# Optimization experiments

Hardware: AMD Instinct MI355X
Metric: run time of the kernel (lower is better)

Reference implementation:

```python
import jax, jax.numpy as jnp
import numpy as np

B, L = 32, 200
NUM_C, NUM_D, DIM_V = 256, 32, 128


def setup_inputs() -> dict:
    key = jax.random.key(0)
    ks = jax.random.split(key, 20)
    def n(k, shape, s=0.05):
        return (jax.random.normal(k, shape) * s).astype(jnp.float32)
    return {
        "c_seq": jax.random.randint(ks[0], (B, L), 0, NUM_C),
        "d_seq": jax.random.randint(ks[1], (B, L), 0, NUM_D),
        "r_seq": jax.random.uniform(ks[2], (B, L), dtype=jnp.float32),
        # learned params
        "X": n(ks[3], (NUM_C * NUM_D, DIM_V), 0.1),      # Embedding table
        "v_r": n(ks[4], (DIM_V,), 0.1),
        "v_beta": n(ks[5], (DIM_V,), 0.1),
        # GRU (torch layout: gates [r|z|n] stacked)
        "W_ih": n(ks[6], (3 * DIM_V, 2 * DIM_V)),
        "W_hh": n(ks[7], (3 * DIM_V, DIM_V)),
        "b_ih": n(ks[8], (3 * DIM_V,)),
        "b_hh": n(ks[9], (3 * DIM_V,)),
        # linear_1: dim_v -> dim_v -> num_d (dropout = identity in eval)
        "W1a": n(ks[10], (DIM_V, DIM_V)), "b1a": n(ks[11], (DIM_V,)),
        "W1b": n(ks[12], (NUM_D, DIM_V)), "b1b": n(ks[13], (NUM_D,)),
        # linear_2: 3*dim_v -> dim_v -> num_d
        "W2a": n(ks[14], (DIM_V, 3 * DIM_V)), "b2a": n(ks[15], (DIM_V,)),
        "W2b": n(ks[16], (NUM_D, DIM_V)), "b2b": n(ks[17], (NUM_D,)),
    }


def reference(c_seq, d_seq, r_seq, X, v_r, v_beta, W_ih, W_hh, b_ih, b_hh,
              W1a, b1a, W1b, b1b, W2a, b2a, W2b, b2b):
    # embedding lookup: x = c + num_c * d
    v_x_seq = X[c_seq + NUM_C * d_seq]              # [B,L,V]
    v_r_seq = r_seq[..., None] * v_r                # [B,L,V]
    gru_in = jnp.concatenate([v_x_seq, v_r_seq], -1)  # [B,L,2V]

    # GRU (torch semantics), precompute input projections
    gx = jnp.einsum('blf,gf->blg', gru_in, W_ih) + b_ih  # [B,L,3V]

    def gru_step(h, gx_t):
        gh = h @ W_hh.T + b_hh
        xr, xz, xn = jnp.split(gx_t, 3, axis=-1)
        hr, hz, hn = jnp.split(gh, 3, axis=-1)
        r = jax.nn.sigmoid(xr + hr)
        z = jax.nn.sigmoid(xz + hz)
        n_ = jnp.tanh(xn + r * hn)
        h = (1.0 - z) * n_ + z * h
        return h, h

    h0 = jnp.zeros((B, DIM_V), dtype=gru_in.dtype)
    _, h_seq = jax.lax.scan(gru_step, h0, jnp.swapaxes(gx, 0, 1))
    h_seq = jnp.swapaxes(h_seq, 0, 1)               # [B,L,V]

    # linear_1 (dropout is identity at inference)
    alpha_seq = jax.nn.relu(h_seq @ W1a.T + b1a) @ W1b.T + b1b  # [B,L,num_d]

    # sequential memory update; one-hot gather/scatter expressed as true
    # gather C[b, c_t, d_t] and row scatter C[b, c_t, :] = new_c (same math)
    bidx = jnp.arange(B)

    def mem_step(C, inp):
        c_t, d_t, vx_t, vr_t = inp
        beta = C[bidx, c_t, d_t]                    # [B]
        v_beta_t = beta[:, None] * v_beta           # [B,V]
        zcat = jnp.concatenate([v_beta_t, vx_t, vr_t], -1)  # [B,3V]
        new_c = jax.nn.relu(zcat @ W2a.T + b2a) @ W2b.T + b2b  # [B,num_d]
        C = C.at[bidx, c_t].set(new_c)
        return C, C

    C0 = jnp.zeros((B, NUM_C, NUM_D), jnp.float32)
    _, C_seq = jax.lax.scan(
        mem_step, C0,
        (jnp.swapaxes(c_seq, 0, 1), jnp.swapaxes(d_seq, 0, 1),
         jnp.swapaxes(v_x_seq, 0, 1), jnp.swapaxes(v_r_seq, 0, 1)))
    C_seq = jnp.swapaxes(C_seq, 0, 1)               # [B,L,num_c,num_d]
    return alpha_seq, h_seq, C_seq
```

## Files before the change

### kernel.cpp

```cpp
#include <hip/hip_runtime.h>
#include <hip/hip_bf16.h>

typedef unsigned short u16;
typedef unsigned int u32;
typedef short short8 __attribute__((ext_vector_type(8)));
typedef float f32x4 __attribute__((ext_vector_type(4)));

constexpr int BATCH = 32, L = 200, NUM_C = 256, NUM_D = 32, V = 128;
constexpr int G3 = 384;
constexpr int KQ = 512;
constexpr int ROWS = BATCH * L;
constexpr size_t ALPHA_OFF = 0;
constexpr size_t H_OFF = (size_t)ROWS * NUM_D;
constexpr size_t C_OFF = H_OFF + (size_t)ROWS * V;

__device__ inline u16 f2bf(float f) {
  __hip_bfloat16 h = __float2bfloat16(f);
  return __builtin_bit_cast(u16, h);
}
__device__ inline float bf2f(u16 u) { u32 x = ((u32)u) << 16; return __builtin_bit_cast(float, x); }

__device__ inline void cvt32(const float* __restrict__ src, u16* __restrict__ dst) {
#pragma unroll
  for (int j0 = 0; j0 < 32; j0 += 4) {
    const f32x4 v = *(const f32x4*)(src + j0);
    ushort4 s;
    s.x = f2bf(v[0]); s.y = f2bf(v[1]); s.z = f2bf(v[2]); s.w = f2bf(v[3]);
    *(ushort4*)(dst + j0) = s;
  }
}
__device__ inline short8 ldfrag(const float* __restrict__ p) {
  const f32x4 a = *(const f32x4*)p, b = *(const f32x4*)(p + 4);
  short8 s;
  s[0] = (short)f2bf(a[0]); s[1] = (short)f2bf(a[1]);
  s[2] = (short)f2bf(a[2]); s[3] = (short)f2bf(a[3]);
  s[4] = (short)f2bf(b[0]); s[5] = (short)f2bf(b[1]);
  s[6] = (short)f2bf(b[2]); s[7] = (short)f2bf(b[3]);
  return s;
}

__global__ __launch_bounds__(256) void k1(
    const int* __restrict__ c_seq, const int* __restrict__ d_seq,
    const float* __restrict__ r_seq, const float* __restrict__ X,
    const float* __restrict__ v_r, const float* __restrict__ W_ih,
    const float* __restrict__ W2a, const float* __restrict__ b_ih,
    const float* __restrict__ b2a, float* __restrict__ Qout)
{
  __shared__ __align__(16) u16 Als[64][144];
  __shared__ __align__(16) u16 Bls[64][144];
  const int tid = threadIdx.x;
  const int mt = blockIdx.x, nt = blockIdx.y;
  const int lane = tid & 63, w = tid >> 6;
  const int q = lane >> 4, m = lane & 15;

  f32x4 acc[4];
#pragma unroll
  for (int i = 0; i < 4; ++i) acc[i] = (f32x4)0.0f;

  const int r0 = tid >> 2;
  const int kc = (tid & 3) * 32;
  const int rowg = mt * 64 + r0;
  const int gcolB = nt * 64 + r0;

  for (int s = 0; s < 2; ++s) {
    if (s) __syncthreads();
    if (s == 0) {
      const int idx = c_seq[rowg] + NUM_C * d_seq[rowg];
      cvt32(X + (size_t)idx * V + kc, &Als[r0][kc]);
    } else {
      const float rv = r_seq[rowg];
#pragma unroll
      for (int j0 = 0; j0 < 32; j0 += 4) {
        const f32x4 v = *(const f32x4*)(v_r + kc + j0);
        ushort4 sv;
        sv.x = f2bf(rv * v[0]); sv.y = f2bf(rv * v[1]);
        sv.z = f2bf(rv * v[2]); sv.w = f2bf(rv * v[3]);
        *(ushort4*)&Als[r0][kc + j0] = sv;
      }
    }
    {
      const float* src = (gcolB < G3)
        ? (W_ih + (size_t)gcolB * 256 + s * 128 + kc)
        : (W2a + (size_t)(gcolB - G3) * G3 + V + s * 128 + kc);
      cvt32(src, &Bls[r0][kc]);
    }
    __syncthreads();
#pragma unroll
    for (int c = 0; c < 4; ++c) {
      const short8 af = *(const short8*)&Als[w * 16 + m][32 * c + 8 * q];
#pragma unroll
      for (int i = 0; i < 4; ++i) {
        const short8 bf = *(const short8*)&Bls[i * 16 + m][32 * c + 8 * q];
        acc[i] = __builtin_amdgcn_mfma_f32_16x16x32_bf16(af, bf, acc[i], 0, 0, 0);
      }
    }
  }
#pragma unroll
  for (int i = 0; i < 4; ++i) {
    const int col = nt * 64 + i * 16 + m;
    const float bias = (col < G3) ? b_ih[col] : b2a[col - G3];
#pragma unroll
    for (int r = 0; r < 4; ++r) {
      const int rowo = mt * 64 + w * 16 + q * 4 + r;
      Qout[(size_t)rowo * KQ + col] = acc[i][r] + bias;
    }
  }
}

union ShK2 {
  struct { u16 h_bf[2][V]; } g;
  struct { float C[NUM_C * NUM_D]; int cb[L]; int db[L]; float u[V]; } s;
};

__global__ __launch_bounds__(256, 1) void k2(
    const int* __restrict__ c_seq, const int* __restrict__ d_seq,
    const float* __restrict__ W_hh, const float* __restrict__ b_hh,
    const float* __restrict__ W2a, const float* __restrict__ v_beta,
    const float* __restrict__ W2b, const float* __restrict__ b2b,
    const float* __restrict__ Q, float* __restrict__ out)
{
  __shared__ __align__(16) ShK2 sh;
  const int tid = threadIdx.x;
  const int l = tid & 63, w = tid >> 6, q = l >> 4, m = l & 15;

  if (blockIdx.x < 32) {
    const int b = blockIdx.x;
    if (tid < V) sh.g.h_bf[0][tid] = 0;
    __syncthreads();
    short8 wf[6][4];
    float bhh[6]; int gcol[6];
#pragma unroll
    for (int i = 0; i < 6; ++i) {
      const int g = (w + 4 * i) * 16 + m;
      gcol[i] = g;
      bhh[i] = b_hh[g];
#pragma unroll
      for (int c = 0; c < 4; ++c)
        wf[i][c] = ldfrag(W_hh + (size_t)g * V + 32 * c + 8 * q);
    }
    const float* Qb = Q + (size_t)b * L * KQ;
    float* outh = out + H_OFF + (size_t)b * L * V;
    const int vi0 = 16 * w + m, vi1 = 64 + 16 * w + m;
    float hold[2] = {0.f, 0.f};
    float hst[2] = {0.f, 0.f};
    float gxv[6];
#pragma unroll
    for (int i = 0; i < 6; ++i) gxv[i] = Qb[gcol[i]];
    for (int t = 0; t < L; ++t) {
      const int rs = t & 1, wsl = rs ^ 1;
      short8 af[4];
#pragma unroll
      for (int c = 0; c < 4; ++c)
        af[c] = *(const short8*)&sh.g.h_bf[rs][32 * c + 8 * q];
      float gxn[6];
      const float* Qn = Qb + (size_t)((t + 1 < L) ? t + 1 : t) * KQ;
#pragma unroll
      for (int i = 0; i < 6; ++i) gxn[i] = Qn[gcol[i]];
      if (t > 0 && q == 0) {
        outh[(size_t)(t - 1) * V + vi0] = hst[0];
        outh[(size_t)(t - 1) * V + vi1] = hst[1];
      }
      f32x4 acc[6];
#pragma unroll
      for (int i = 0; i < 6; ++i) acc[i] = (f32x4)0.0f;
#pragma unroll
      for (int c = 0; c < 4; ++c)
#pragma unroll
        for (int i = 0; i < 6; ++i)
          acc[i] = __builtin_amdgcn_mfma_f32_16x16x32_bf16(af[c], wf[i][c], acc[i], 0, 0, 0);
      float hnew[2];
#pragma unroll
      for (int s = 0; s < 2; ++s) {
        const float xr = gxv[0 + s] + acc[0 + s][0] + bhh[0 + s];
        const float xz = gxv[2 + s] + acc[2 + s][0] + bhh[2 + s];
        const float ghn = acc[4 + s][0] + bhh[4 + s];
        const float r = 1.f / (1.f + __expf(-xr));
        const float z = 1.f / (1.f + __expf(-xz));
        const float xn = gxv[4 + s] + r * ghn;
        const float e = __expf(2.f * xn);
        const float n = 1.f - 2.f / (e + 1.f);
        hnew[s] = (1.f - z) * n + z * hold[s];
      }
      if (q == 0) {
        sh.g.h_bf[wsl][vi0] = f2bf(hnew[0]);
        sh.g.h_bf[wsl][vi1] = f2bf(hnew[1]);
      }
      hold[0] = hnew[0]; hold[1] = hnew[1];
      hst[0] = hnew[0]; hst[1] = hnew[1];
      __builtin_amdgcn_s_waitcnt(0xc07f);
      __builtin_amdgcn_s_barrier();
#pragma unroll
      for (int i = 0; i < 6; ++i) gxv[i] = gxn[i];
    }
    if (q == 0) {
      outh[(size_t)(L - 1) * V + vi0] = hst[0];
      outh[(size_t)(L - 1) * V + vi1] = hst[1];
    }
  } else {
    const int b = blockIdx.x - 32;
    for (int i = tid; i < NUM_C * NUM_D; i += 256) sh.s.C[i] = 0.f;
    if (tid < L) { sh.s.cb[tid] = c_seq[b * L + tid]; sh.s.db[tid] = d_seq[b * L + tid]; }
    if (tid < V) {
      float a = 0.f;
      const float* wr = W2a + (size_t)tid * G3;
      for (int k = 0; k < V; ++k) a += wr[k] * v_beta[k];
      sh.s.u[tid] = a;
    }
    __syncthreads();
    if (tid >= 64) return;
    float ureg[4][8];
#pragma unroll
    for (int c = 0; c < 4; ++c)
#pragma unroll
      for (int j = 0; j < 8; ++j) ureg[c][j] = sh.s.u[32 * c + 8 * q + j];
    short8 wbf[2][4];
    float bb[2];
#pragma unroll
    for (int tt = 0; tt < 2; ++tt) {
#pragma unroll
      for (int c = 0; c < 4; ++c)
        wbf[tt][c] = ldfrag(W2b + (size_t)(tt * 16 + m) * V + 32 * c + 8 * q);
      bb[tt] = b2b[tt * 16 + m];
    }
    const float* Pb = Q + (size_t)b * L * KQ + G3;
    float* outc = out + C_OFF + (size_t)b * L * (NUM_C * NUM_D);
    f32x4 pcur[4][2];
#pragma unroll
    for (int c = 0; c < 4; ++c) {
      pcur[c][0] = *(const f32x4*)(Pb + 32 * c + 8 * q);
      pcur[c][1] = *(const f32x4*)(Pb + 32 * c + 8 * q + 4);
    }
    float beta = 0.f;
    int ct = sh.s.cb[0];
    for (int t = 0; t < L; ++t) {
      __builtin_amdgcn_s_waitcnt(0xc07f);
      const int tn = (t + 1 < L) ? t + 1 : t;
      const int cn = sh.s.cb[tn], dn = sh.s.db[tn];
      const float bpre = sh.s.C[cn * NUM_D + dn];
      short8 af[4];
#pragma unroll
      for (int c = 0; c < 4; ++c) {
        short8 a;
#pragma unroll
        for (int j = 0; j < 8; ++j) {
          const float p = (j < 4) ? pcur[c][0][j] : pcur[c][1][j - 4];
          const float hv = fmaxf(beta * ureg[c][j] + p, 0.f);
          a[j] = (short)f2bf(hv);
        }
        af[c] = a;
      }
      const float* Pn = Pb + (size_t)tn * KQ;
#pragma unroll
      for (int c = 0; c < 4; ++c) {
        pcur[c][0] = *(const f32x4*)(Pn + 32 * c + 8 * q);
        pcur[c][1] = *(const f32x4*)(Pn + 32 * c + 8 * q + 4);
      }
      f32x4 a0 = (f32x4)0.0f, a1 = (f32x4)0.0f;
#pragma unroll
      for (int c = 0; c < 4; ++c) {
        a0 = __builtin_amdgcn_mfma_f32_16x16x32_bf16(af[c], wbf[0][c], a0, 0, 0, 0);
        a1 = __builtin_amdgcn_mfma_f32_16x16x32_bf16(af[c], wbf[1][c], a1, 0, 0, 0);
      }
      const float n0 = a0[0] + bb[0], n1 = a1[0] + bb[1];
      if (q == 0) {
        sh.s.C[ct * NUM_D + m] = n0;
        sh.s.C[ct * NUM_D + 16 + m] = n1;
        float* oc = outc + (size_t)t * (NUM_C * NUM_D) + ct * NUM_D;
        oc[m] = n0;
        oc[16 + m] = n1;
      }
      float nb = bpre;
      if (cn == ct) nb = (dn < 16) ? __shfl(n0, dn, 64) : __shfl(n1, dn - 16, 64);
      beta = nb;
      ct = cn;
    }
  }
}

union ShK3 {
  struct { int cb[L]; float stage[L][NUM_D]; } f;
  struct { u16 hls[64][144]; u16 hid[64][144]; } a;
};

__global__ __launch_bounds__(256) void k3(
    const int* __restrict__ c_seq, const float* __restrict__ W1a,
    const float* __restrict__ b1a, const float* __restrict__ W1b,
    const float* __restrict__ b1b, float* __restrict__ out)
{
  __shared__ __align__(16) ShK3 sh;
  const int tid = threadIdx.x;
  if (blockIdx.x < 256) {
    const int blk = blockIdx.x;
    const int b = blk >> 3, cbase = (blk & 7) * 32;
    if (tid < L) sh.f.cb[tid] = c_seq[b * L + tid];
    __syncthreads();
    if (tid < L) {
      const int c = sh.f.cb[tid];
      if (c >= cbase && c < cbase + 32) {
        const float* src = out + C_OFF + ((size_t)b * L + tid) * (NUM_C * NUM_D) + (size_t)c * NUM_D;
#pragma unroll
        for (int j = 0; j < 8; ++j)
          *(f32x4*)&sh.f.stage[tid][j * 4] = *(const f32x4*)(src + j * 4);
      }
    }
    __syncthreads();
    const int cl = tid >> 3, dq = (tid & 7) * 4;
    const int myc = cbase + cl;
    float* base = out + C_OFF + (size_t)b * L * (NUM_C * NUM_D) + (size_t)myc * NUM_D + dq;
    f32x4 cur = (f32x4)0.0f;
    for (int t = 0; t < L; ++t) {
      if (sh.f.cb[t] == myc) cur = *(const f32x4*)&sh.f.stage[t][dq];
      *(f32x4*)base = cur;
      base += NUM_C * NUM_D;
    }
  } else {
    const int ab = blockIdx.x - 256;
    const int l = tid & 63, w = tid >> 6, q = l >> 4, m = l & 15;
    {
      const int r0 = tid >> 2, kc = (tid & 3) * 32;
      cvt32(out + H_OFF + (size_t)(ab * 64 + r0) * V + kc, &sh.a.hls[r0][kc]);
    }
    __syncthreads();
    f32x4 acc1[8];
#pragma unroll
    for (int i = 0; i < 8; ++i) acc1[i] = (f32x4)0.0f;
#pragma unroll
    for (int c = 0; c < 4; ++c) {
      const short8 af = *(const short8*)&sh.a.hls[w * 16 + m][32 * c + 8 * q];
#pragma unroll
      for (int i = 0; i < 8; ++i) {
        const short8 bf = ldfrag(W1a + (size_t)(i * 16 + m) * V + 32 * c + 8 * q);
        acc1[i] = __builtin_amdgcn_mfma_f32_16x16x32_bf16(af, bf, acc1[i], 0, 0, 0);
      }
    }
#pragma unroll
    for (int i = 0; i < 8; ++i) {
      const int col = i * 16 + m;
      const float bias = b1a[col];
#pragma unroll
      for (int r = 0; r < 4; ++r)
        sh.a.hid[w * 16 + q * 4 + r][col] = f2bf(fmaxf(acc1[i][r] + bias, 0.f));
    }
    __syncthreads();
    f32x4 acc2[2];
    acc2[0] = (f32x4)0.0f; acc2[1] = (f32x4)0.0f;
#pragma unroll
    for (int c = 0; c < 4; ++c) {
      const short8 af = *(const short8*)&sh.a.hid[w * 16 + m][32 * c + 8 * q];
#pragma unroll
      for (int tt = 0; tt < 2; ++tt) {
        const short8 bf = ldfrag(W1b + (size_t)(tt * 16 + m) * V + 32 * c + 8 * q);
        acc2[tt] = __builtin_amdgcn_mfma_f32_16x16x32_bf16(af, bf, acc2[tt], 0, 0, 0);
      }
    }
#pragma unroll
    for (int tt = 0; tt < 2; ++tt) {
      const int col = tt * 16 + m;
      const float bias = b1b[col];
#pragma unroll
      for (int r = 0; r < 4; ++r) {
        const int row = ab * 64 + w * 16 + q * 4 + r;
        out[ALPHA_OFF + (size_t)row * NUM_D + col] = acc2[tt][r] + bias;
      }
    }
  }
}

extern "C" void kernel_launch(void* const* d_in, const int* in_sizes, int n_in,
                              void* d_out, int out_size, void* d_ws, size_t ws_size,
                              hipStream_t stream) {
  const int*   c_seq  = (const int*)d_in[0];
  const int*   d_seq  = (const int*)d_in[1];
  const float* r_seq  = (const float*)d_in[2];
  const float* X      = (const float*)d_in[3];
  const float* v_r    = (const float*)d_in[4];
  const float* v_beta = (const float*)d_in[5];
  const float* W_ih   = (const float*)d_in[6];
  const float* W_hh   = (const float*)d_in[7];
  const float* b_ih   = (const float*)d_in[8];
  const float* b_hh   = (const float*)d_in[9];
  const float* W1a    = (const float*)d_in[10];
  const float* b1a    = (const float*)d_in[11];
  const float* W1b    = (const float*)d_in[12];
  const float* b1b    = (const float*)d_in[13];
  const float* W2a    = (const float*)d_in[14];
  const float* b2a    = (const float*)d_in[15];
  const float* W2b    = (const float*)d_in[16];
  const float* b2b    = (const float*)d_in[17];
  float* out = (float*)d_out;
  float* Q = (float*)d_ws;

  k1<<<dim3(100, 8), 256, 0, stream>>>(c_seq, d_seq, r_seq, X, v_r, W_ih, W2a, b_ih, b2a, Q);
  k2<<<64, 256, 0, stream>>>(c_seq, d_seq, W_hh, b_hh, W2a, v_beta, W2b, b2b, Q, out);
  k3<<<356, 256, 0, stream>>>(c_seq, W1a, b1a, W1b, b1b, out);
}
```

Measured before the change: 401.7 us.

## Split C-seq fill over time chunks and break GRU MFMA accumulation chains

The k3 C-sequence fill kernel now splits each (batch, c-group) over four time chunks of 50 steps, giving 1024 blocks instead of 256. Each chunk recovers its starting row value by scanning backward for the last earlier write and reading it from global memory. This raises parallelism for the large C output write, at the cost of redundant c_seq scans. Separately, the GRU recurrence now uses four independent MFMA accumulators per gate tile and sums them afterwards, shortening the dependent MFMA chain on the serial critical path.

```diff
diff --git a/kernel.cpp b/kernel.cpp
--- a/kernel.cpp
+++ b/kernel.cpp
@@ -10,6 +10,7 @@
 constexpr int G3 = 384;
 constexpr int KQ = 512;
 constexpr int ROWS = BATCH * L;
+constexpr int TCH = 50;
 constexpr size_t ALPHA_OFF = 0;
 constexpr size_t H_OFF = (size_t)ROWS * NUM_D;
 constexpr size_t C_OFF = H_OFF + (size_t)ROWS * V;
@@ -160,20 +161,26 @@
         outh[(size_t)(t - 1) * V + vi0] = hst[0];
         outh[(size_t)(t - 1) * V + vi1] = hst[1];
       }
-      f32x4 acc[6];
-#pragma unroll
-      for (int i = 0; i < 6; ++i) acc[i] = (f32x4)0.0f;
+      f32x4 acc[6][4];
+#pragma unroll
+      for (int i = 0; i < 6; ++i)
+#pragma unroll
+        for (int c = 0; c < 4; ++c) acc[i][c] = (f32x4)0.0f;
 #pragma unroll
       for (int c = 0; c < 4; ++c)
 #pragma unroll
         for (int i = 0; i < 6; ++i)
-          acc[i] = __builtin_amdgcn_mfma_f32_16x16x32_bf16(af[c], wf[i][c], acc[i], 0, 0, 0);
+          acc[i][c] = __builtin_amdgcn_mfma_f32_16x16x32_bf16(af[c], wf[i][c], acc[i][c], 0, 0, 0);
+      float gh[6];
+#pragma unroll
+      for (int i = 0; i < 6; ++i)
+        gh[i] = (acc[i][0][0] + acc[i][1][0]) + (acc[i][2][0] + acc[i][3][0]);
       float hnew[2];
 #pragma unroll
       for (int s = 0; s < 2; ++s) {
-        const float xr = gxv[0 + s] + acc[0 + s][0] + bhh[0 + s];
-        const float xz = gxv[2 + s] + acc[2 + s][0] + bhh[2 + s];
-        const float ghn = acc[4 + s][0] + bhh[4 + s];
+        const float xr = gxv[0 + s] + gh[0 + s] + bhh[0 + s];
+        const float xz = gxv[2 + s] + gh[2 + s] + bhh[2 + s];
+        const float ghn = gh[4 + s] + bhh[4 + s];
         const float r = 1.f / (1.f + __expf(-xr));
         const float z = 1.f / (1.f + __expf(-xz));
         const float xn = gxv[4 + s] + r * ghn;
@@ -278,7 +285,7 @@
 }
 
 union ShK3 {
-  struct { int cb[L]; float stage[L][NUM_D]; } f;
+  struct { int cb[L]; int bnd[32]; float stage[TCH][NUM_D]; } f;
   struct { u16 hls[64][144]; u16 hid[64][144]; } a;
 };
 
@@ -289,32 +296,43 @@
 {
   __shared__ __align__(16) ShK3 sh;
   const int tid = threadIdx.x;
-  if (blockIdx.x < 256) {
+  if (blockIdx.x < 1024) {
     const int blk = blockIdx.x;
-    const int b = blk >> 3, cbase = (blk & 7) * 32;
+    const int tc = blk & 3, cg = (blk >> 2) & 7, b = blk >> 5;
+    const int t0 = tc * TCH, cbase = cg * 32;
     if (tid < L) sh.f.cb[tid] = c_seq[b * L + tid];
     __syncthreads();
-    if (tid < L) {
-      const int c = sh.f.cb[tid];
+    if (tid < TCH) {
+      const int t = t0 + tid;
+      const int c = sh.f.cb[t];
       if (c >= cbase && c < cbase + 32) {
-        const float* src = out + C_OFF + ((size_t)b * L + tid) * (NUM_C * NUM_D) + (size_t)c * NUM_D;
+        const float* src = out + C_OFF + ((size_t)b * L + t) * (NUM_C * NUM_D) + (size_t)c * NUM_D;
 #pragma unroll
         for (int j = 0; j < 8; ++j)
           *(f32x4*)&sh.f.stage[tid][j * 4] = *(const f32x4*)(src + j * 4);
       }
     }
+    if (tid < 32) {
+      int found = -1;
+      for (int t = t0 - 1; t >= 0; --t)
+        if (sh.f.cb[t] == cbase + tid) { found = t; break; }
+      sh.f.bnd[tid] = found;
+    }
     __syncthreads();
     const int cl = tid >> 3, dq = (tid & 7) * 4;
     const int myc = cbase + cl;
-    float* base = out + C_OFF + (size_t)b * L * (NUM_C * NUM_D) + (size_t)myc * NUM_D + dq;
     f32x4 cur = (f32x4)0.0f;
-    for (int t = 0; t < L; ++t) {
-      if (sh.f.cb[t] == myc) cur = *(const f32x4*)&sh.f.stage[t][dq];
+    const int bt = sh.f.bnd[cl];
+    if (bt >= 0)
+      cur = *(const f32x4*)(out + C_OFF + ((size_t)b * L + bt) * (NUM_C * NUM_D) + (size_t)myc * NUM_D + dq);
+    float* base = out + C_OFF + ((size_t)b * L + t0) * (NUM_C * NUM_D) + (size_t)myc * NUM_D + dq;
+    for (int t = t0; t < t0 + TCH; ++t) {
+      if (sh.f.cb[t] == myc) cur = *(const f32x4*)&sh.f.stage[t - t0][dq];
       *(f32x4*)base = cur;
       base += NUM_C * NUM_D;
     }
   } else {
-    const int ab = blockIdx.x - 256;
+    const int ab = blockIdx.x - 1024;
     const int l = tid & 63, w = tid >> 6, q = l >> 4, m = l & 15;
     {
       const int r0 = tid >> 2, kc = (tid & 3) * 32;
@@ -392,5 +410,5 @@
 
   k1<<<dim3(100, 8), 256, 0, stream>>>(c_seq, d_seq, r_seq, X, v_r, W_ih, W2a, b_ih, b2a, Q);
   k2<<<64, 256, 0, stream>>>(c_seq, d_seq, W_hh, b_hh, W2a, v_beta, W2b, b2b, Q, out);
-  k3<<<356, 256, 0, stream>>>(c_seq, W1a, b1a, W1b, b1b, out);
-}
+  k3<<<1124, 256, 0, stream>>>(c_seq, W1a, b1a, W1b, b1b, out);
+}
```

New measurement: 425.5 us. 1.06x slower.

## Run GRU recurrence with two waves per block and two-step gx prefetch

Applied to the files above, without the earlier changes.

The GRU recurrence block shrinks from four to two wavefronts. Each wave now holds twelve W_hh fragments and computes four hidden outputs per step, which should make the per-step barrier cheaper and cut cross-wave coordination. The gx input projections are prefetched two timesteps ahead using alternating register buffers, to hide global load latency behind the MFMA chain. The cost is more serial MFMA and gate work per wave and higher register pressure. The memory-update blocks now also run with 128 threads, and their setup loops were adjusted to match.

```diff
diff --git a/kernel.cpp b/kernel.cpp
--- a/kernel.cpp
+++ b/kernel.cpp
@@ -112,7 +112,7 @@
   struct { float C[NUM_C * NUM_D]; int cb[L]; int db[L]; float u[V]; } s;
 };
 
-__global__ __launch_bounds__(256, 1) void k2(
+__global__ __launch_bounds__(128, 1) void k2(
     const int* __restrict__ c_seq, const int* __restrict__ d_seq,
     const float* __restrict__ W_hh, const float* __restrict__ b_hh,
     const float* __restrict__ W2a, const float* __restrict__ v_beta,
@@ -125,13 +125,15 @@
 
   if (blockIdx.x < 32) {
     const int b = blockIdx.x;
-    if (tid < V) sh.g.h_bf[0][tid] = 0;
-    __syncthreads();
-    short8 wf[6][4];
-    float bhh[6]; int gcol[6];
-#pragma unroll
-    for (int i = 0; i < 6; ++i) {
-      const int g = (w + 4 * i) * 16 + m;
+    sh.g.h_bf[0][tid] = 0;
+    __syncthreads();
+    short8 wf[12][4];
+    float bhh[12]; int gcol[12]; int hp[4];
+#pragma unroll
+    for (int tt = 0; tt < 4; ++tt) hp[tt] = w * 64 + tt * 16 + m;
+#pragma unroll
+    for (int i = 0; i < 12; ++i) {
+      const int g = (i >> 2) * 128 + w * 64 + (i & 3) * 16 + m;
       gcol[i] = g;
       bhh[i] = b_hh[g];
 #pragma unroll
@@ -140,67 +142,79 @@
     }
     const float* Qb = Q + (size_t)b * L * KQ;
     float* outh = out + H_OFF + (size_t)b * L * V;
-    const int vi0 = 16 * w + m, vi1 = 64 + 16 * w + m;
-    float hold[2] = {0.f, 0.f};
-    float hst[2] = {0.f, 0.f};
-    float gxv[6];
-#pragma unroll
-    for (int i = 0; i < 6; ++i) gxv[i] = Qb[gcol[i]];
-    for (int t = 0; t < L; ++t) {
+    const f32x4 z4 = (f32x4)0.0f;
+    float hold[4] = {0.f, 0.f, 0.f, 0.f};
+    float hst[4] = {0.f, 0.f, 0.f, 0.f};
+    float gxA[12], gxB[12];
+#pragma unroll
+    for (int i = 0; i < 12; ++i) gxA[i] = Qb[gcol[i]];
+#pragma unroll
+    for (int i = 0; i < 12; ++i) gxB[i] = Qb[KQ + gcol[i]];
+
+    auto step = [&](int t, float (&gx)[12]) {
       const int rs = t & 1, wsl = rs ^ 1;
       short8 af[4];
 #pragma unroll
       for (int c = 0; c < 4; ++c)
         af[c] = *(const short8*)&sh.g.h_bf[rs][32 * c + 8 * q];
-      float gxn[6];
-      const float* Qn = Qb + (size_t)((t + 1 < L) ? t + 1 : t) * KQ;
-#pragma unroll
-      for (int i = 0; i < 6; ++i) gxn[i] = Qn[gcol[i]];
       if (t > 0 && q == 0) {
-        outh[(size_t)(t - 1) * V + vi0] = hst[0];
-        outh[(size_t)(t - 1) * V + vi1] = hst[1];
-      }
-      f32x4 acc[6];
-#pragma unroll
-      for (int i = 0; i < 6; ++i) acc[i] = (f32x4)0.0f;
-#pragma unroll
-      for (int c = 0; c < 4; ++c)
-#pragma unroll
-        for (int i = 0; i < 6; ++i)
+#pragma unroll
+        for (int tt = 0; tt < 4; ++tt)
+          outh[(size_t)(t - 1) * V + hp[tt]] = hst[tt];
+      }
+      f32x4 acc[12];
+#pragma unroll
+      for (int i = 0; i < 12; ++i)
+        acc[i] = __builtin_amdgcn_mfma_f32_16x16x32_bf16(af[0], wf[i][0], z4, 0, 0, 0);
+#pragma unroll
+      for (int c = 1; c < 4; ++c)
+#pragma unroll
+        for (int i = 0; i < 12; ++i)
           acc[i] = __builtin_amdgcn_mfma_f32_16x16x32_bf16(af[c], wf[i][c], acc[i], 0, 0, 0);
-      float hnew[2];
-#pragma unroll
-      for (int s = 0; s < 2; ++s) {
-        const float xr = gxv[0 + s] + acc[0 + s][0] + bhh[0 + s];
-        const float xz = gxv[2 + s] + acc[2 + s][0] + bhh[2 + s];
-        const float ghn = acc[4 + s][0] + bhh[4 + s];
+      float hnew[4];
+#pragma unroll
+      for (int tt = 0; tt < 4; ++tt) {
+        const float xr = gx[tt] + acc[tt][0] + bhh[tt];
+        const float xz = gx[4 + tt] + acc[4 + tt][0] + bhh[4 + tt];
+        const float ghn = acc[8 + tt][0] + bhh[8 + tt];
         const float r = 1.f / (1.f + __expf(-xr));
         const float z = 1.f / (1.f + __expf(-xz));
-        const float xn = gxv[4 + s] + r * ghn;
+        const float xn = gx[8 + tt] + r * ghn;
         const float e = __expf(2.f * xn);
         const float n = 1.f - 2.f / (e + 1.f);
-        hnew[s] = (1.f - z) * n + z * hold[s];
+        hnew[tt] = (1.f - z) * n + z * hold[tt];
       }
       if (q == 0) {
-        sh.g.h_bf[wsl][vi0] = f2bf(hnew[0]);
-        sh.g.h_bf[wsl][vi1] = f2bf(hnew[1]);
-      }
-      hold[0] = hnew[0]; hold[1] = hnew[1];
-      hst[0] = hnew[0]; hst[1] = hnew[1];
+#pragma unroll
+        for (int tt = 0; tt < 4; ++tt)
+          sh.g.h_bf[wsl][hp[tt]] = f2bf(hnew[tt]);
+      }
+#pragma unroll
+      for (int tt = 0; tt < 4; ++tt) { hold[tt] = hnew[tt]; hst[tt] = hnew[tt]; }
+      const int tr = (t + 2 < L) ? t + 2 : L - 1;
+      const float* Qr = Qb + (size_t)tr * KQ;
+#pragma unroll
+      for (int i = 0; i < 12; ++i) gx[i] = Qr[gcol[i]];
       __builtin_amdgcn_s_waitcnt(0xc07f);
       __builtin_amdgcn_s_barrier();
-#pragma unroll
-      for (int i = 0; i < 6; ++i) gxv[i] = gxn[i];
+    };
+
+    for (int t = 0; t < L; t += 2) {
+      step(t, gxA);
+      step(t + 1, gxB);
     }
     if (q == 0) {
-      outh[(size_t)(L - 1) * V + vi0] = hst[0];
-      outh[(size_t)(L - 1) * V + vi1] = hst[1];
+#pragma unroll
+      for (int tt = 0; tt < 4; ++tt)
+        outh[(size_t)(L - 1) * V + hp[tt]] = hst[tt];
     }
   } else {
     const int b = blockIdx.x - 32;
-    for (int i = tid; i < NUM_C * NUM_D; i += 256) sh.s.C[i] = 0.f;
-    if (tid < L) { sh.s.cb[tid] = c_seq[b * L + tid]; sh.s.db[tid] = d_seq[b * L + tid]; }
-    if (tid < V) {
+    for (int i = tid; i < NUM_C * NUM_D; i += 128) sh.s.C[i] = 0.f;
+    for (int i = tid; i < L; i += 128) {
+      sh.s.cb[i] = c_seq[b * L + i]; sh.s.db[i] = d_seq[b * L + i];
+    }
+    {
       float a = 0.f;
       const float* wr = W2a + (size_t)tid * G3;
       for (int k = 0; k < V; ++k) a += wr[k] * v_beta[k];
@@ -391,6 +405,6 @@
   float* Q = (float*)d_ws;
 
   k1<<<dim3(100, 8), 256, 0, stream>>>(c_seq, d_seq, r_seq, X, v_r, W_ih, W2a, b_ih, b2a, Q);
-  k2<<<64, 256, 0, stream>>>(c_seq, d_seq, W_hh, b_hh, W2a, v_beta, W2b, b2b, Q, out);
+  k2<<<64, 128, 0, stream>>>(c_seq, d_seq, W_hh, b_hh, W2a, v_beta, W2b, b2b, Q, out);
   k3<<<356, 256, 0, stream>>>(c_seq, W1a, b1a, W1b, b1b, out);
 }
```

Result: slower. 472.3 us (+17.6%).
